# Kernel optimization log

Hardware: AMD Instinct MI355X
Metric: run time of the kernel (lower is better)

The kernel has to match this reference:

```python
import jax, jax.numpy as jnp
import numpy as np

WS = 8          # window size
DIM = 512       # midplanes
HEADS = 16      # 512 // 32
HD = DIM // HEADS
SCALE = HD ** -0.5
EPS = 1e-5      # BatchNorm eps


def _rel_index():
    # Swin-style relative position index, (WS*WS, WS*WS) int32, static.
    coords = np.stack(np.meshgrid(np.arange(WS), np.arange(WS), indexing='ij')).reshape(2, -1)
    rel = (coords[:, :, None] - coords[:, None, :]).transpose(1, 2, 0)
    rel[..., 0] += WS - 1
    rel[..., 1] += WS - 1
    rel[..., 0] *= 2 * WS - 1
    return jnp.asarray(rel.sum(-1), dtype=jnp.int32)

REL_IDX = _rel_index()


def _bn(x, gamma, beta, mean, var):
    # eval-mode BatchNorm2d on (B, C, H, W)
    inv = jax.lax.rsqrt(var + EPS)
    return (x - mean[None, :, None, None]) * (inv * gamma)[None, :, None, None] + beta[None, :, None, None]


def _forward(x, qkv_w, qkv_b, proj_w, proj_b, rel_bias_table,
             bn1_gamma, bn1_beta, bn1_mean, bn1_var,
             mlp_w1, mlp_b1, mlp_w2, mlp_b2,
             bn2_gamma, bn2_beta, bn2_mean, bn2_var):
    B, C, H, W = x.shape
    Hb, Wb = H // WS, W // WS
    shortcut = x

    xn = _bn(x, bn1_gamma, bn1_beta, bn1_mean, bn1_var)

    # window_partition (islocal=True): (B,C,H,W) -> (B*nW, WS*WS, C)
    xw = xn.reshape(B, C, Hb, WS, Wb, WS).transpose(0, 2, 4, 3, 5, 1).reshape(-1, WS * WS, C)

    # WindowAttention
    B_, N, _ = xw.shape
    qkv = xw @ qkv_w + qkv_b                       # (B_, N, 3*C)
    qkv = qkv.reshape(B_, N, 3, HEADS, HD).transpose(2, 0, 3, 1, 4)
    q, k, v = qkv[0], qkv[1], qkv[2]               # (B_, H, N, HD)
    attn = jnp.einsum('bhnd,bhmd->bhnm', q * SCALE, k)
    bias = rel_bias_table[REL_IDX]                 # (N, N, HEADS)
    attn = attn + bias.transpose(2, 0, 1)[None]
    attn = jax.nn.softmax(attn, axis=-1)
    out = jnp.einsum('bhnm,bhmd->bhnd', attn, v).transpose(0, 2, 1, 3).reshape(B_, N, C)
    out = out @ proj_w + proj_b                    # (B_, N, C)

    # window_reverse (islocal=True) — replicate torch's .view reinterpretation exactly
    aw = out.reshape(-1, WS, WS, DIM)              # (B*nW, WS, WS, C) contiguous
    xr = aw.reshape(B, DIM, Hb, Wb, WS, WS)        # row-major reinterpret (as in torch .view)
    xr = xr.transpose(0, 1, 2, 4, 3, 5).reshape(B, DIM, H, W)

    x1 = shortcut + xr                             # drop_path is identity at eval

    # MLP of 1x1 convs
    xn2 = _bn(x1, bn2_gamma, bn2_beta, bn2_mean, bn2_var)
    h = jnp.einsum('oc,bchw->bohw', mlp_w1, xn2) + mlp_b1[None, :, None, None]
    h = jax.nn.gelu(h, approximate=False)
    h = jnp.einsum('oc,bchw->bohw', mlp_w2, h) + mlp_b2[None, :, None, None]
    return x1 + h


def setup_inputs() -> dict:
    key = jax.random.key(0)
    ks = jax.random.split(key, 12)
    B, H, W = 8, 128, 128
    s = 0.02
    return {
        'x': jax.random.normal(ks[0], (B, DIM, H, W), dtype=jnp.float32),
        'qkv_w': jax.random.normal(ks[1], (DIM, 3 * DIM), dtype=jnp.float32) * s,
        'qkv_b': jnp.zeros((3 * DIM,), jnp.float32),
        'proj_w': jax.random.normal(ks[2], (DIM, DIM), dtype=jnp.float32) * s,
        'proj_b': jnp.zeros((DIM,), jnp.float32),
        'rel_bias_table': jax.random.normal(ks[3], ((2 * WS - 1) ** 2, HEADS), dtype=jnp.float32) * s,
        'bn1_gamma': jnp.ones((DIM,), jnp.float32),
        'bn1_beta': jnp.zeros((DIM,), jnp.float32),
        'bn1_mean': jax.random.normal(ks[4], (DIM,), dtype=jnp.float32) * 0.1,
        'bn1_var': jax.random.uniform(ks[5], (DIM,), jnp.float32, 0.5, 1.5),
        'mlp_w1': jax.random.normal(ks[6], (DIM, DIM), dtype=jnp.float32) * s,
        'mlp_b1': jnp.zeros((DIM,), jnp.float32),
        'mlp_w2': jax.random.normal(ks[7], (DIM, DIM), dtype=jnp.float32) * s,
        'mlp_b2': jnp.zeros((DIM,), jnp.float32),
        'bn2_gamma': jnp.ones((DIM,), jnp.float32),
        'bn2_beta': jnp.zeros((DIM,), jnp.float32),
        'bn2_mean': jax.random.normal(ks[8], (DIM,), dtype=jnp.float32) * 0.1,
        'bn2_var': jax.random.uniform(ks[9], (DIM,), jnp.float32, 0.5, 1.5),
    }


def reference(x, qkv_w, qkv_b, proj_w, proj_b, rel_bias_table,
              bn1_gamma, bn1_beta, bn1_mean, bn1_var,
              mlp_w1, mlp_b1, mlp_w2, mlp_b2,
              bn2_gamma, bn2_beta, bn2_mean, bn2_var):
    return _forward(x, qkv_w, qkv_b, proj_w, proj_b, rel_bias_table,
                    bn1_gamma, bn1_beta, bn1_mean, bn1_var,
                    mlp_w1, mlp_b1, mlp_w2, mlp_b2,
                    bn2_gamma, bn2_beta, bn2_mean, bn2_var)
```

## Files before the change

kernel.cpp:

```cpp
#include <hip/hip_runtime.h>
#include <cstddef>


typedef unsigned short ushort_t;
typedef __attribute__((ext_vector_type(8))) short short8;
typedef __attribute__((ext_vector_type(4))) float float4v;

__device__ __forceinline__ float bf2f(unsigned short h) {
  union { unsigned int u; float f; } c; c.u = ((unsigned int)h) << 16; return c.f;
}
__device__ __forceinline__ unsigned short f2bf(float f) {
  union { float f; unsigned int u; } c; c.f = f;
  unsigned int u = c.u;
  unsigned int r = u + 0x7fffu + ((u >> 16) & 1u);
  return (unsigned short)(r >> 16);
}
__device__ __forceinline__ void async16(const void* g, void* l) {
  __builtin_amdgcn_global_load_lds(
      (const __attribute__((address_space(1))) unsigned int*)g,
      (__attribute__((address_space(3))) unsigned int*)l, 16, 0, 0);
}

#define BAR() asm volatile("s_barrier" ::: "memory")
#define WAITV6() asm volatile("s_waitcnt vmcnt(6)" ::: "memory")
#define WAITV0() asm volatile("s_waitcnt vmcnt(0)" ::: "memory")

__global__ void transpose_cast(const float* __restrict__ W, ushort_t* __restrict__ Wt,
                               int K, int N) {
  int idx = blockIdx.x * 256 + threadIdx.x;
  if (idx >= K * N) return;
  int nn = idx / K, kk = idx - nn * K;
  Wt[idx] = f2bf(W[(size_t)kk * N + nn]);
}
__global__ void cast_bf(const float* __restrict__ W, ushort_t* __restrict__ Wt, int total) {
  int idx = blockIdx.x * 256 + threadIdx.x;
  if (idx < total) Wt[idx] = f2bf(W[idx]);
}

__global__ __launch_bounds__(256) void prep_qkv(
    const float* __restrict__ x, const float* __restrict__ gamma,
    const float* __restrict__ beta, const float* __restrict__ mean,
    const float* __restrict__ var, ushort_t* __restrict__ A0) {
  const int w = blockIdx.x;
  const int cc0 = blockIdx.y << 5;
  const int b = w >> 8, hb = (w >> 4) & 15, wb = w & 15;
  __shared__ __align__(16) ushort_t tile[64][32];
  const int tid = threadIdx.x;
  const int ci = tid >> 3, row = tid & 7;
  const int c = cc0 + ci;
  const float a = gamma[c] * rsqrtf(var[c] + 1e-5f);
  const float sh = beta[c] - mean[c] * a;
  const float* xp = x + (((size_t)b * 512 + c) * 128 + (hb << 3) + row) * 128 + (wb << 3);
#pragma unroll
  for (int j = 0; j < 8; ++j) tile[(row << 3) + j][ci] = f2bf(xp[j] * a + sh);
  __syncthreads();
  const int n = tid >> 2, d0 = (tid & 3) << 3;
  *(uint4*)(A0 + (size_t)((w << 6) + n) * 512 + cc0 + d0) = *(const uint4*)&tile[n][d0];
}

#define QUAD(BB, MH, NH)                                                        \
  __builtin_amdgcn_s_setprio(1);                                                \
  _Pragma("unroll")                                                             \
  for (int mi = 0; mi < 4; ++mi) {                                              \
    _Pragma("unroll")                                                           \
    for (int nj = 0; nj < 2; ++nj) {                                            \
      _Pragma("unroll")                                                         \
      for (int kk = 0; kk < 2; ++kk)                                            \
        acc[(MH * 4) + mi][(NH * 2) + nj] =                                     \
            __builtin_amdgcn_mfma_f32_16x16x32_bf16(                            \
                a[mi][kk], BB[nj][kk], acc[(MH * 4) + mi][(NH * 2) + nj], 0, 0, 0); \
    }                                                                           \
  }                                                                             \
  __builtin_amdgcn_s_setprio(0);

template <int EPI>
__global__ __launch_bounds__(512, 2) void gemm256(
    const ushort_t* __restrict__ A, const ushort_t* __restrict__ Bt,
    const float* __restrict__ bias, ushort_t* __restrict__ C,
    int M, int N, int K) {
  __shared__ __align__(16) ushort_t smem[65536];
  ushort_t* A0L = smem;
  ushort_t* B0L = smem + 16384;
  ushort_t* A1L = smem + 32768;
  ushort_t* B1L = smem + 49152;

  const int tid = threadIdx.x;
  const int wid = tid >> 6, lane = tid & 63;

  const int gx = gridDim.x;
  const int nwg = gx * gridDim.y;
  const int orig = blockIdx.y * gx + blockIdx.x;
  const int q = nwg >> 3, r = nwg & 7;
  const int xcd = orig & 7, lid = orig >> 3;
  const int swz = (xcd < r ? xcd * (q + 1) : r * (q + 1) + (xcd - r) * q) + lid;
  const int by = swz / gx, bx = swz - by * gx;
  const int m0 = by << 8, n0 = bx << 8;

  const int NT = K >> 6;
  const int NI = NT >> 1;

  const int sseg = (lane & 7) ^ (lane >> 3);
  auto stA = [&](ushort_t* dst, int stripe, int kt) {
#pragma unroll
    for (int j = 0; j < 2; ++j) {
      const int pr = (j << 7) + (stripe << 6) + (wid << 3);
      async16(A + (size_t)(m0 + pr + (lane >> 3)) * K + (kt << 6) + (sseg << 3),
              dst + ((size_t)pr << 6));
    }
  };
  auto stB = [&](ushort_t* dst, int stripe, int kt) {
#pragma unroll
    for (int j = 0; j < 2; ++j) {
      const int pr = (j << 7) + ((wid >> 2) << 6) + (stripe << 5) + ((wid & 3) << 3);
      async16(Bt + (size_t)(n0 + pr + (lane >> 3)) * K + (kt << 6) + (sseg << 3),
              dst + ((size_t)pr << 6));
    }
  };

  const int fr = lane & 15, kg = lane >> 4;
  const int wr = wid >> 2, wc = wid & 3;
  const int ar0 = (wr << 7) + fr;
  const int br0 = (wc << 6) + fr;
  const int sx = fr & 7;
  auto ldA = [&](const ushort_t* buf, int mi_abs, int kk) -> short8 {
    const int row = ar0 + (mi_abs << 4);
    const int seg = ((kk << 2) + kg) ^ sx;
    return *(const short8*)(buf + (row << 6) + (seg << 3));
  };
  auto ldB = [&](const ushort_t* buf, int ni_abs, int kk) -> short8 {
    const int row = br0 + (ni_abs << 4);
    const int seg = ((kk << 2) + kg) ^ sx;
    return *(const short8*)(buf + (row << 6) + (seg << 3));
  };

  short8 a[4][2], b0[2][2], b1[2][2];
  float4v acc[8][4];
#pragma unroll
  for (int i = 0; i < 8; ++i)
#pragma unroll
    for (int j = 0; j < 4; ++j)
#pragma unroll
      for (int rr = 0; rr < 4; ++rr) acc[i][j][rr] = 0.0f;

  stA(A0L, 0, 0);
  stB(B0L, 0, 0);
  stB(B0L, 1, 0);
  stA(A0L, 1, 0);
  stA(A1L, 0, 1);
  stB(B1L, 1, 1);
  stA(A1L, 1, 1);
  WAITV6();
  BAR();

  for (int i = 0; i < NI; ++i) {
    const int ktB = 2 * i + 1;
    const int kt2 = 2 * i + 2, kt3 = 2 * i + 3;
    const bool st = (kt2 < NT);
#pragma unroll
    for (int mi = 0; mi < 4; ++mi) { a[mi][0] = ldA(A0L, mi, 0); a[mi][1] = ldA(A0L, mi, 1); }
#pragma unroll
    for (int nj = 0; nj < 2; ++nj) { b0[nj][0] = ldB(B0L, nj, 0); b0[nj][1] = ldB(B0L, nj, 1); }
    stB(B1L, 0, ktB);
    BAR();
    QUAD(b0, 0, 0);
    BAR();
#pragma unroll
    for (int nj = 0; nj < 2; ++nj) { b1[nj][0] = ldB(B0L, 2 + nj, 0); b1[nj][1] = ldB(B0L, 2 + nj, 1); }
    if (st) stA(A0L, 0, kt2);
    BAR();
    QUAD(b1, 0, 1);
    BAR();
#pragma unroll
    for (int mi = 0; mi < 4; ++mi) { a[mi][0] = ldA(A0L, 4 + mi, 0); a[mi][1] = ldA(A0L, 4 + mi, 1); }
    if (st) stB(B0L, 1, kt2);
    BAR();
    QUAD(b1, 1, 1);
    BAR();
    if (st) stA(A0L, 1, kt2);
    BAR();
    QUAD(b0, 1, 0);
    if (st) { WAITV6(); } else { WAITV0(); }
    BAR();
#pragma unroll
    for (int mi = 0; mi < 4; ++mi) { a[mi][0] = ldA(A1L, mi, 0); a[mi][1] = ldA(A1L, mi, 1); }
#pragma unroll
    for (int nj = 0; nj < 2; ++nj) { b0[nj][0] = ldB(B1L, nj, 0); b0[nj][1] = ldB(B1L, nj, 1); }
    if (st) stB(B0L, 0, kt2);
    BAR();
    QUAD(b0, 0, 0);
    BAR();
#pragma unroll
    for (int nj = 0; nj < 2; ++nj) { b1[nj][0] = ldB(B1L, 2 + nj, 0); b1[nj][1] = ldB(B1L, 2 + nj, 1); }
    if (st) stA(A1L, 0, kt3);
    BAR();
    QUAD(b1, 0, 1);
    BAR();
#pragma unroll
    for (int mi = 0; mi < 4; ++mi) { a[mi][0] = ldA(A1L, 4 + mi, 0); a[mi][1] = ldA(A1L, 4 + mi, 1); }
    if (st) stB(B1L, 1, kt3);
    BAR();
    QUAD(b1, 1, 1);
    BAR();
    if (st) stA(A1L, 1, kt3);
    BAR();
    QUAD(b0, 1, 0);
    if (st) { WAITV6(); }
    BAR();
  }

  const int cr = kg << 2;
#pragma unroll
  for (int ni = 0; ni < 4; ++ni) {
    const int col = n0 + (wc << 6) + (ni << 4) + fr;
    const float bv = bias[col];
#pragma unroll
    for (int mi = 0; mi < 8; ++mi) {
      const size_t base = (size_t)(m0 + (wr << 7) + (mi << 4) + cr) * N + col;
#pragma unroll
      for (int rr = 0; rr < 4; ++rr) {
        float v = acc[mi][ni][rr] + bv;
        if (EPI == 1) v = 0.5f * v * (1.0f + erff(v * 0.70710678118654752f));
        C[base + (size_t)rr * N] = f2bf(v);
      }
    }
  }
}

__global__ __launch_bounds__(256) void attn_kernel(
    const ushort_t* __restrict__ QKV, const float* __restrict__ table,
    ushort_t* __restrict__ OUT) {
  const int w = blockIdx.x;
  const int h = blockIdx.y;
  __shared__ __align__(16) ushort_t Vt[32][72];
  __shared__ __align__(16) ushort_t Pw[4][16][72];
  __shared__ float bias_s[225];
  const int tid = threadIdx.x;
  const int wave = tid >> 6, lane = tid & 63;
  const int g = lane >> 4, c = lane & 15;

  if (tid < 225) bias_s[tid] = table[tid * 16 + h];

  const ushort_t* base = QKV + (size_t)(w << 6) * 1536 + h * 32;

  {
    uint4 vv = *(const uint4*)(base + (size_t)lane * 1536 + 1024 + (wave << 3));
    const ushort_t* vp = (const ushort_t*)&vv;
#pragma unroll
    for (int e = 0; e < 8; ++e) Vt[(wave << 3) + e][lane] = vp[e];
  }

  short8 qf = *(const short8*)(base + (size_t)((wave << 4) + c) * 1536 + (g << 3));
  short8 kf[4];
#pragma unroll
  for (int j = 0; j < 4; ++j)
    kf[j] = *(const short8*)(base + (size_t)((j << 4) + c) * 1536 + 512 + (g << 3));

  float4v acc[4];
#pragma unroll
  for (int j = 0; j < 4; ++j) {
#pragma unroll
    for (int r = 0; r < 4; ++r) acc[j][r] = 0.0f;
    acc[j] = __builtin_amdgcn_mfma_f32_16x16x32_bf16(qf, kf[j], acc[j], 0, 0, 0);
  }

  __syncthreads();

  const int q0 = (wave << 4) + (g << 2);
#pragma unroll
  for (int j = 0; j < 4; ++j) {
    const int k = (j << 4) + c;
    const int r2 = k >> 3, c2 = k & 7;
#pragma unroll
    for (int r = 0; r < 4; ++r) {
      const int qq = q0 + r;
      const int idx = ((qq >> 3) - r2 + 7) * 15 + ((qq & 7) - c2 + 7);
      acc[j][r] = acc[j][r] * 0.17677669529663689f + bias_s[idx];
    }
  }

#pragma unroll
  for (int r = 0; r < 4; ++r) {
    float m = fmaxf(fmaxf(acc[0][r], acc[1][r]), fmaxf(acc[2][r], acc[3][r]));
    m = fmaxf(m, __shfl_xor(m, 1));
    m = fmaxf(m, __shfl_xor(m, 2));
    m = fmaxf(m, __shfl_xor(m, 4));
    m = fmaxf(m, __shfl_xor(m, 8));
    float s = 0.0f;
#pragma unroll
    for (int j = 0; j < 4; ++j) { acc[j][r] = __expf(acc[j][r] - m); s += acc[j][r]; }
    s += __shfl_xor(s, 1);
    s += __shfl_xor(s, 2);
    s += __shfl_xor(s, 4);
    s += __shfl_xor(s, 8);
    const float inv = 1.0f / s;
#pragma unroll
    for (int j = 0; j < 4; ++j)
      Pw[wave][(g << 2) + r][(j << 4) + c] = f2bf(acc[j][r] * inv);
  }

  __syncthreads();

  float4v oacc[2];
#pragma unroll
  for (int j2 = 0; j2 < 2; ++j2)
#pragma unroll
    for (int r = 0; r < 4; ++r) oacc[j2][r] = 0.0f;
#pragma unroll
  for (int ks = 0; ks < 2; ++ks) {
    short8 pa = *(const short8*)&Pw[wave][c][(ks << 5) + (g << 3)];
#pragma unroll
    for (int j2 = 0; j2 < 2; ++j2) {
      short8 vb = *(const short8*)&Vt[(j2 << 4) + c][(ks << 5) + (g << 3)];
      oacc[j2] = __builtin_amdgcn_mfma_f32_16x16x32_bf16(pa, vb, oacc[j2], 0, 0, 0);
    }
  }

  ushort_t* op = OUT + (size_t)((w << 6) + (wave << 4)) * 512 + h * 32;
#pragma unroll
  for (int j2 = 0; j2 < 2; ++j2)
#pragma unroll
    for (int r = 0; r < 4; ++r)
      op[(size_t)((g << 2) + r) * 512 + (j2 << 4) + c] = f2bf(oacc[j2][r]);
}

__device__ __forceinline__ size_t scramble_idx(int b, int F) {
  const int hb0 = F >> 19, wb0 = (F >> 15) & 15;
  const int rr = (F >> 12) & 7, ccol = (F >> 9) & 7, ch = F & 511;
  return ((size_t)(b * 256 + hb0 * 16 + wb0) * 64 + rr * 8 + ccol) * 512 + ch;
}

__global__ __launch_bounds__(256) void prep_mlp(
    const float* __restrict__ x, const ushort_t* __restrict__ PROJ,
    const float* __restrict__ gamma, const float* __restrict__ beta,
    const float* __restrict__ mean, const float* __restrict__ var,
    ushort_t* __restrict__ XN2) {
  const int pc = blockIdx.x;
  const int cc0 = blockIdx.y << 5;
  const int p0 = pc << 6;
  const int b = p0 >> 14, hh = (p0 >> 7) & 127;
  __shared__ __align__(16) ushort_t tile[64][32];
  const int tid = threadIdx.x;
  const int ci = tid >> 3, wg = (tid & 7) << 3;
  const int c = cc0 + ci;
  const float a = gamma[c] * rsqrtf(var[c] + 1e-5f);
  const float sh = beta[c] - mean[c] * a;
  const int w0 = (p0 & 127) + wg;
  const float* xp = x + (((size_t)b * 512 + c) * 128 + hh) * 128 + w0;
  const int hb = hh >> 3, r2 = hh & 7;
#pragma unroll
  for (int j = 0; j < 8; ++j) {
    const int ww = w0 + j;
    const int F = (c << 14) + (hb << 10) + ((ww >> 3) << 6) + (r2 << 3) + (ww & 7);
    const float x1 = xp[j] + bf2f(PROJ[scramble_idx(b, F)]);
    tile[wg + j][ci] = f2bf(x1 * a + sh);
  }
  __syncthreads();
  const int i2 = tid >> 2, d0 = (tid & 3) << 3;
  *(uint4*)(XN2 + (size_t)(p0 + i2) * 512 + cc0 + d0) = *(const uint4*)&tile[i2][d0];
}

__global__ __launch_bounds__(256) void final_add(
    const float* __restrict__ x, const ushort_t* __restrict__ PROJ,
    const ushort_t* __restrict__ H2, float* __restrict__ out) {
  const int pc = blockIdx.x, cc0 = blockIdx.y << 5;
  const int p0 = pc << 6;
  const int b = p0 >> 14, hh = (p0 >> 7) & 127;
  __shared__ float tile[32][65];
  const int tid = threadIdx.x;
  {
    const int i2 = tid >> 2, d0 = (tid & 3) << 3;
    const ushort_t* hp = H2 + (size_t)(p0 + i2) * 512 + cc0 + d0;
#pragma unroll
    for (int j = 0; j < 8; ++j) tile[d0 + j][i2] = bf2f(hp[j]);
  }
  __syncthreads();
  const int ci = tid >> 3, wg = (tid & 7) << 3;
  const int c = cc0 + ci;
  const int w0 = (p0 & 127) + wg;
  const float* xp = x + (((size_t)b * 512 + c) * 128 + hh) * 128 + w0;
  float* op = out + (((size_t)b * 512 + c) * 128 + hh) * 128 + w0;
  const int hb = hh >> 3, r2 = hh & 7;
#pragma unroll
  for (int j = 0; j < 8; ++j) {
    const int ww = w0 + j;
    const int F = (c << 14) + (hb << 10) + ((ww >> 3) << 6) + (r2 << 3) + (ww & 7);
    op[j] = xp[j] + bf2f(PROJ[scramble_idx(b, F)]) + tile[ci][wg + j];
  }
}

extern "C" void kernel_launch(void* const* d_in, const int* in_sizes, int n_in,
                              void* d_out, int out_size, void* d_ws, size_t ws_size,
                              hipStream_t stream) {
  const float* x      = (const float*)d_in[0];
  const float* qkv_w  = (const float*)d_in[1];
  const float* qkv_b  = (const float*)d_in[2];
  const float* proj_w = (const float*)d_in[3];
  const float* proj_b = (const float*)d_in[4];
  const float* rel_t  = (const float*)d_in[5];
  const float* bn1g = (const float*)d_in[6];
  const float* bn1b = (const float*)d_in[7];
  const float* bn1m = (const float*)d_in[8];
  const float* bn1v = (const float*)d_in[9];
  const float* w1 = (const float*)d_in[10];
  const float* b1 = (const float*)d_in[11];
  const float* w2 = (const float*)d_in[12];
  const float* b2 = (const float*)d_in[13];
  const float* bn2g = (const float*)d_in[14];
  const float* bn2b = (const float*)d_in[15];
  const float* bn2m = (const float*)d_in[16];
  const float* bn2v = (const float*)d_in[17];
  float* out = (float*)d_out;

  char* ws = (char*)d_ws;
  const size_t SZ = (size_t)131072 * 512 * 2;
  ushort_t* WQKV  = (ushort_t*)(ws);
  ushort_t* WPROJ = (ushort_t*)(ws + 1572864);
  ushort_t* W1B   = (ushort_t*)(ws + 2097152);
  ushort_t* W2B   = (ushort_t*)(ws + 2621440);
  ushort_t* A0    = (ushort_t*)(ws + 3145728);
  ushort_t* QKV   = (ushort_t*)(ws + 3145728 + SZ);
  ushort_t* OUTB  = A0;
  ushort_t* PROJ  = QKV;
  ushort_t* XN2   = (ushort_t*)((char*)QKV + SZ);
  ushort_t* H1    = (ushort_t*)((char*)QKV + 2 * SZ);
  ushort_t* H2    = A0;

  transpose_cast<<<(512 * 1536 + 255) / 256, 256, 0, stream>>>(qkv_w, WQKV, 512, 1536);
  transpose_cast<<<(512 * 512 + 255) / 256, 256, 0, stream>>>(proj_w, WPROJ, 512, 512);
  cast_bf<<<(512 * 512 + 255) / 256, 256, 0, stream>>>(w1, W1B, 512 * 512);
  cast_bf<<<(512 * 512 + 255) / 256, 256, 0, stream>>>(w2, W2B, 512 * 512);

  prep_qkv<<<dim3(2048, 16), 256, 0, stream>>>(x, bn1g, bn1b, bn1m, bn1v, A0);
  gemm256<0><<<dim3(6, 512), 512, 0, stream>>>(A0, WQKV, qkv_b, QKV, 131072, 1536, 512);
  attn_kernel<<<dim3(2048, 16), 256, 0, stream>>>(QKV, rel_t, OUTB);
  gemm256<0><<<dim3(2, 512), 512, 0, stream>>>(OUTB, WPROJ, proj_b, PROJ, 131072, 512, 512);
  prep_mlp<<<dim3(2048, 16), 256, 0, stream>>>(x, PROJ, bn2g, bn2b, bn2m, bn2v, XN2);
  gemm256<1><<<dim3(2, 512), 512, 0, stream>>>(XN2, W1B, b1, H1, 131072, 512, 512);
  gemm256<0><<<dim3(2, 512), 512, 0, stream>>>(H1, W2B, b2, H2, 131072, 512, 512);
  final_add<<<dim3(2048, 16), 256, 0, stream>>>(x, PROJ, H2, out);
}
```

Measured before the change: 1.750 ms.

## Scatter proj GEMM output to NCHW layout so consumers read contiguously

```diff
diff --git a/kernel.cpp b/kernel.cpp
--- a/kernel.cpp
+++ b/kernel.cpp
@@ -100,20 +100,20 @@
   const int NI = NT >> 1;
 
   const int sseg = (lane & 7) ^ (lane >> 3);
+  const ushort_t* Agl = A + (size_t)(m0 + (lane >> 3)) * K + (sseg << 3);
+  const ushort_t* Bgl = Bt + (size_t)(n0 + (lane >> 3)) * K + (sseg << 3);
   auto stA = [&](ushort_t* dst, int stripe, int kt) {
 #pragma unroll
     for (int j = 0; j < 2; ++j) {
       const int pr = (j << 7) + (stripe << 6) + (wid << 3);
-      async16(A + (size_t)(m0 + pr + (lane >> 3)) * K + (kt << 6) + (sseg << 3),
-              dst + ((size_t)pr << 6));
+      async16(Agl + pr * K + (kt << 6), dst + (pr << 6));
     }
   };
   auto stB = [&](ushort_t* dst, int stripe, int kt) {
 #pragma unroll
     for (int j = 0; j < 2; ++j) {
       const int pr = (j << 7) + ((wid >> 2) << 6) + (stripe << 5) + ((wid & 3) << 3);
-      async16(Bt + (size_t)(n0 + pr + (lane >> 3)) * K + (kt << 6) + (sseg << 3),
-              dst + ((size_t)pr << 6));
+      async16(Bgl + pr * K + (kt << 6), dst + (pr << 6));
     }
   };
 
@@ -209,18 +209,40 @@
   }
 
   const int cr = kg << 2;
-#pragma unroll
-  for (int ni = 0; ni < 4; ++ni) {
-    const int col = n0 + (wc << 6) + (ni << 4) + fr;
-    const float bv = bias[col];
-#pragma unroll
-    for (int mi = 0; mi < 8; ++mi) {
-      const size_t base = (size_t)(m0 + (wr << 7) + (mi << 4) + cr) * N + col;
-#pragma unroll
-      for (int rr = 0; rr < 4; ++rr) {
-        float v = acc[mi][ni][rr] + bv;
-        if (EPI == 1) v = 0.5f * v * (1.0f + erff(v * 0.70710678118654752f));
-        C[base + (size_t)rr * N] = f2bf(v);
+  if (EPI == 2) {
+#pragma unroll
+    for (int ni = 0; ni < 4; ++ni) {
+      const int ch = n0 + (wc << 6) + (ni << 4) + fr;
+      const float bv = bias[ch];
+      const int hlow = (ch >> 3) & 7;
+      const int wmw = ((ch >> 6) & 7) << 3 | (ch & 7);
+#pragma unroll
+      for (int mi = 0; mi < 8; ++mi) {
+#pragma unroll
+        for (int rr = 0; rr < 4; ++rr) {
+          const int m = m0 + (wr << 7) + (mi << 4) + cr + rr;
+          const int b = m >> 14, tp = m & 16383;
+          const int c = ((tp >> 6) << 1) | ((tp >> 5) & 1);
+          const int h = (((tp >> 1) & 15) << 3) | hlow;
+          const int w = ((tp & 1) << 6) | wmw;
+          C[((size_t)(b * 512 + c) << 14) + (h << 7) + w] = f2bf(acc[mi][ni][rr] + bv);
+        }
+      }
+    }
+  } else {
+#pragma unroll
+    for (int ni = 0; ni < 4; ++ni) {
+      const int col = n0 + (wc << 6) + (ni << 4) + fr;
+      const float bv = bias[col];
+#pragma unroll
+      for (int mi = 0; mi < 8; ++mi) {
+        const size_t base = (size_t)(m0 + (wr << 7) + (mi << 4) + cr) * N + col;
+#pragma unroll
+        for (int rr = 0; rr < 4; ++rr) {
+          float v = acc[mi][ni][rr] + bv;
+          if (EPI == 1) v = 0.5f * v * (1.0f + erff(v * 0.70710678118654752f));
+          C[base + (size_t)rr * N] = f2bf(v);
+        }
       }
     }
   }
@@ -323,14 +345,8 @@
       op[(size_t)((g << 2) + r) * 512 + (j2 << 4) + c] = f2bf(oacc[j2][r]);
 }
 
-__device__ __forceinline__ size_t scramble_idx(int b, int F) {
-  const int hb0 = F >> 19, wb0 = (F >> 15) & 15;
-  const int rr = (F >> 12) & 7, ccol = (F >> 9) & 7, ch = F & 511;
-  return ((size_t)(b * 256 + hb0 * 16 + wb0) * 64 + rr * 8 + ccol) * 512 + ch;
-}
-
 __global__ __launch_bounds__(256) void prep_mlp(
-    const float* __restrict__ x, const ushort_t* __restrict__ PROJ,
+    const float* __restrict__ x, const ushort_t* __restrict__ PROJ2,
     const float* __restrict__ gamma, const float* __restrict__ beta,
     const float* __restrict__ mean, const float* __restrict__ var,
     ushort_t* __restrict__ XN2) {
@@ -345,13 +361,13 @@
   const float a = gamma[c] * rsqrtf(var[c] + 1e-5f);
   const float sh = beta[c] - mean[c] * a;
   const int w0 = (p0 & 127) + wg;
-  const float* xp = x + (((size_t)b * 512 + c) * 128 + hh) * 128 + w0;
-  const int hb = hh >> 3, r2 = hh & 7;
+  const size_t off = (((size_t)b * 512 + c) * 128 + hh) * 128 + w0;
+  const float* xp = x + off;
+  uint4 pv = *(const uint4*)(PROJ2 + off);
+  const ushort_t* pu = (const ushort_t*)&pv;
 #pragma unroll
   for (int j = 0; j < 8; ++j) {
-    const int ww = w0 + j;
-    const int F = (c << 14) + (hb << 10) + ((ww >> 3) << 6) + (r2 << 3) + (ww & 7);
-    const float x1 = xp[j] + bf2f(PROJ[scramble_idx(b, F)]);
+    const float x1 = xp[j] + bf2f(pu[j]);
     tile[wg + j][ci] = f2bf(x1 * a + sh);
   }
   __syncthreads();
@@ -360,7 +376,7 @@
 }
 
 __global__ __launch_bounds__(256) void final_add(
-    const float* __restrict__ x, const ushort_t* __restrict__ PROJ,
+    const float* __restrict__ x, const ushort_t* __restrict__ PROJ2,
     const ushort_t* __restrict__ H2, float* __restrict__ out) {
   const int pc = blockIdx.x, cc0 = blockIdx.y << 5;
   const int p0 = pc << 6;
@@ -377,15 +393,14 @@
   const int ci = tid >> 3, wg = (tid & 7) << 3;
   const int c = cc0 + ci;
   const int w0 = (p0 & 127) + wg;
-  const float* xp = x + (((size_t)b * 512 + c) * 128 + hh) * 128 + w0;
-  float* op = out + (((size_t)b * 512 + c) * 128 + hh) * 128 + w0;
-  const int hb = hh >> 3, r2 = hh & 7;
-#pragma unroll
-  for (int j = 0; j < 8; ++j) {
-    const int ww = w0 + j;
-    const int F = (c << 14) + (hb << 10) + ((ww >> 3) << 6) + (r2 << 3) + (ww & 7);
-    op[j] = xp[j] + bf2f(PROJ[scramble_idx(b, F)]) + tile[ci][wg + j];
-  }
+  const size_t off = (((size_t)b * 512 + c) * 128 + hh) * 128 + w0;
+  const float* xp = x + off;
+  float* op = out + off;
+  uint4 pv = *(const uint4*)(PROJ2 + off);
+  const ushort_t* pu = (const ushort_t*)&pv;
+#pragma unroll
+  for (int j = 0; j < 8; ++j)
+    op[j] = xp[j] + bf2f(pu[j]) + tile[ci][wg + j];
 }
 
 extern "C" void kernel_launch(void* const* d_in, const int* in_sizes, int n_in,
@@ -420,7 +435,7 @@
   ushort_t* A0    = (ushort_t*)(ws + 3145728);
   ushort_t* QKV   = (ushort_t*)(ws + 3145728 + SZ);
   ushort_t* OUTB  = A0;
-  ushort_t* PROJ  = QKV;
+  ushort_t* PROJ2 = QKV;
   ushort_t* XN2   = (ushort_t*)((char*)QKV + SZ);
   ushort_t* H1    = (ushort_t*)((char*)QKV + 2 * SZ);
   ushort_t* H2    = A0;
@@ -433,9 +448,9 @@
   prep_qkv<<<dim3(2048, 16), 256, 0, stream>>>(x, bn1g, bn1b, bn1m, bn1v, A0);
   gemm256<0><<<dim3(6, 512), 512, 0, stream>>>(A0, WQKV, qkv_b, QKV, 131072, 1536, 512);
   attn_kernel<<<dim3(2048, 16), 256, 0, stream>>>(QKV, rel_t, OUTB);
-  gemm256<0><<<dim3(2, 512), 512, 0, stream>>>(OUTB, WPROJ, proj_b, PROJ, 131072, 512, 512);
-  prep_mlp<<<dim3(2048, 16), 256, 0, stream>>>(x, PROJ, bn2g, bn2b, bn2m, bn2v, XN2);
+  gemm256<2><<<dim3(2, 512), 512, 0, stream>>>(OUTB, WPROJ, proj_b, PROJ2, 131072, 512, 512);
+  prep_mlp<<<dim3(2048, 16), 256, 0, stream>>>(x, PROJ2, bn2g, bn2b, bn2m, bn2v, XN2);
   gemm256<1><<<dim3(2, 512), 512, 0, stream>>>(XN2, W1B, b1, H1, 131072, 512, 512);
   gemm256<0><<<dim3(2, 512), 512, 0, stream>>>(H1, W2B, b2, H2, 131072, 512, 512);
-  final_add<<<dim3(2048, 16), 256, 0, stream>>>(x, PROJ, H2, out);
-}
+  final_add<<<dim3(2048, 16), 256, 0, stream>>>(x, PROJ2, H2, out);
+}
```

New measurement: 1.707 ms. 2.4% less time.
